# Optimization experiments

Measured on AMD Instinct MI355X. Metric: run time of the kernel, lower is better.

The kernel has to match this reference:

```python
import jax, jax.numpy as jnp
import numpy as np

N, E, G = 30000, 240000, 1000
F, H = 78, 10            # in-features, GAT heads
HID = F * H              # 780
NEG_SLOPE = 0.2


def setup_inputs() -> dict:
    key = jax.random.key(0)
    ks = jax.random.split(key, 12)
    x = jax.random.normal(ks[0], (N, F), dtype=jnp.float32)
    edge_index = jax.random.randint(ks[1], (2, E), 0, N, dtype=jnp.int32)
    batch = jnp.sort(jax.random.randint(ks[2], (N,), 0, G, dtype=jnp.int32))
    def lin(k, fan_in, shape):
        return (jax.random.normal(k, shape, dtype=jnp.float32)
                / jnp.sqrt(jnp.float32(fan_in)))
    return {
        "x": x,
        "edge_index": edge_index,
        "batch": batch,
        "W_gat": lin(ks[3], F, (F, HID)),          # GATConv lin weight
        "att_src": lin(ks[4], F, (H, F)),          # GAT attention vectors
        "att_dst": lin(ks[5], F, (H, F)),
        "b_gat": jnp.zeros((HID,), jnp.float32),
        "W_gcn": lin(ks[6], HID, (HID, HID)),
        "b_gcn": jnp.zeros((HID,), jnp.float32),
        "W1": lin(ks[7], 2 * HID, (2 * HID, 1500)),
        "b1": jnp.zeros((1500,), jnp.float32),
        "W2": lin(ks[8], 1500, (1500, 128)),
        "b2": jnp.zeros((128,), jnp.float32),
    }


def _with_self_loops(edge_index):
    loop = jnp.arange(N, dtype=edge_index.dtype)
    src = jnp.concatenate([edge_index[0], loop])
    dst = jnp.concatenate([edge_index[1], loop])
    return src, dst


def reference(x, edge_index, batch, W_gat, att_src, att_dst, b_gat,
              W_gcn, b_gcn, W1, b1, W2, b2):
    src, dst = _with_self_loops(edge_index)  # [E+N]

    # ---- GATConv(78 -> 78, heads=10, concat) ----
    h = (x @ W_gat).reshape(N, H, F)                       # [N,H,F]
    a_src = jnp.einsum('nhf,hf->nh', h, att_src)           # [N,H]
    a_dst = jnp.einsum('nhf,hf->nh', h, att_dst)
    e = jax.nn.leaky_relu(a_src[src] + a_dst[dst], NEG_SLOPE)  # [Et,H]
    # segment softmax over incoming edges of each dst node
    e_max = jax.ops.segment_max(e, dst, num_segments=N)
    e_exp = jnp.exp(e - e_max[dst])
    denom = jax.ops.segment_sum(e_exp, dst, num_segments=N)
    alpha = e_exp / denom[dst]                             # [Et,H]
    msg = h[src] * alpha[:, :, None]                       # [Et,H,F]
    out = jax.ops.segment_sum(msg, dst, num_segments=N).reshape(N, HID) + b_gat
    out = jax.nn.relu(out)

    # ---- GCNConv(780 -> 780), symmetric norm with self loops ----
    h2 = out @ W_gcn                                       # [N,HID]
    deg = jax.ops.segment_sum(jnp.ones_like(dst, jnp.float32), dst,
                              num_segments=N)
    dinv = jax.lax.rsqrt(jnp.maximum(deg, 1.0))
    norm = dinv[src] * dinv[dst]                           # [Et]
    out2 = jax.ops.segment_sum(norm[:, None] * h2[src], dst,
                               num_segments=N) + b_gcn
    out2 = jax.nn.relu(out2)

    # ---- global mean / max pool over molecules ----
    counts = jax.ops.segment_sum(jnp.ones((N,), jnp.float32), batch,
                                 num_segments=G)
    gsum = jax.ops.segment_sum(out2, batch, num_segments=G)
    gmean = gsum / jnp.maximum(counts, 1.0)[:, None]
    gmax = jax.ops.segment_max(out2, batch, num_segments=G)
    gmax = jnp.where(counts[:, None] > 0, gmax, 0.0)
    pooled = jnp.concatenate([gmean, gmax], axis=1)        # [G, 1560]

    # ---- MLP head (dropout = identity at eval) ----
    hidfc = jax.nn.relu(pooled @ W1 + b1)
    return hidfc @ W2 + b2                                 # [G, 128]
```

## Files before the change

kernel.cpp:

```cpp
#include <hip/hip_runtime.h>

#define NN 30000
#define EE 240000
#define ET 270000
#define GG 1000
#define NH 10
#define FF 78
#define HID 780
#define NEG_SLOPE 0.2f

#define LD_H 784
#define KP_GCN 832
#define NP_HID 896
#define KP_X 96
#define MP_N 30080
#define KP_P 1568
#define NP_W1 1536
#define LD_FC 1504
#define MP_G 1024

#define MT 128
#define NT 128
#define NBLK 30

typedef __bf16 bf16_8 __attribute__((ext_vector_type(8)));
typedef float f32x4 __attribute__((ext_vector_type(4)));

__device__ __forceinline__ void async_copy16(const void* g, void* l) {
  __builtin_amdgcn_global_load_lds(
      (const __attribute__((address_space(1))) void*)g,
      (__attribute__((address_space(3))) void*)l, 16, 0, 0);
}

__device__ __forceinline__ float bf2f(unsigned int bits) {
  return __uint_as_float(bits << 16);
}

__global__ void init_kernel(int* __restrict__ cnt, int* __restrict__ fill,
                            int* __restrict__ lo, int* __restrict__ hi) {
  int i = blockIdx.x * blockDim.x + threadIdx.x;
  if (i < NN) { cnt[i] = 0; fill[i] = 0; }
  if (i < GG) { lo[i] = NN; hi[i] = 0; }
}

template <bool OUT_BF, int KBC>
__global__ __launch_bounds__(256) void mfma_gemm(
    const __bf16* __restrict__ A, const __bf16* __restrict__ BT,
    float* __restrict__ Cf, __bf16* __restrict__ Cb,
    const float* __restrict__ bias, int M, int Kp, int Nout, int ldc,
    int relu, int rp, int nct, int mtiles) {
  constexpr int NCH = KBC / 8;
  constexpr int TST = KBC / 16;
  constexpr int NST = KBC / 32;
  __shared__ __bf16 As[NCH][MT][8];
  __shared__ __bf16 Bs[NCH][NT][8];
  int rt, ct;
  if (rp > 0) {
    int bid = blockIdx.x;
    int p = bid & 7, s = bid >> 3;
    int q = s / nct;
    rt = p * rp + q;
    ct = s - q * nct;
    if (rt >= mtiles) return;
  } else {
    rt = blockIdx.y; ct = blockIdx.x;
  }
  int row0 = rt * MT, col0 = ct * NT;
  int tid = threadIdx.x;
  int lane = tid & 63, wave = tid >> 6;
  int wm = (wave & 1) * 64, wn = (wave >> 1) * 64;
  int l15 = lane & 15, quad = lane >> 4;
  f32x4 acc[4][4] = {};

  for (int k0 = 0; k0 < Kp; k0 += KBC) {
    for (int t = 0; t < TST; t++) {
      int base = t * 256 + wave * 64;
      int s = base + lane;
      int kc = s >> 7, r = s & 127;
      const __bf16* g = A + (size_t)(row0 + r) * Kp + k0 + kc * 8;
      async_copy16(g, (char*)&As[0][0][0] + (size_t)base * 16);
    }
    for (int t = 0; t < TST; t++) {
      int base = t * 256 + wave * 64;
      int s = base + lane;
      int kc = s >> 7, r = s & 127;
      const __bf16* g = BT + (size_t)(col0 + r) * Kp + k0 + kc * 8;
      async_copy16(g, (char*)&Bs[0][0][0] + (size_t)base * 16);
    }
    __syncthreads();

    bf16_8 af[NST][4], bfv[NST][4];
    for (int st = 0; st < NST; st++) {
      for (int mt = 0; mt < 4; mt++)
        af[st][mt] = *(const bf16_8*)&As[st * 4 + quad][wm + mt * 16 + l15][0];
      for (int nt = 0; nt < 4; nt++)
        bfv[st][nt] = *(const bf16_8*)&Bs[st * 4 + quad][wn + nt * 16 + l15][0];
    }
    for (int st = 0; st < NST; st++)
      for (int mt = 0; mt < 4; mt++)
        for (int nt = 0; nt < 4; nt++)
          acc[mt][nt] = __builtin_amdgcn_mfma_f32_16x16x32_bf16(
              af[st][mt], bfv[st][nt], acc[mt][nt], 0, 0, 0);
    __syncthreads();
  }

  for (int nt = 0; nt < 4; nt++) {
    int col = col0 + wn + nt * 16 + l15;
    if (col >= ldc) continue;
    bool valid = col < Nout;
    float bv = (valid && bias) ? bias[col] : 0.f;
    for (int mt = 0; mt < 4; mt++) {
      int rbase = row0 + wm + mt * 16 + quad * 4;
      for (int r = 0; r < 4; r++) {
        int row = rbase + r;
        if (row >= M) continue;
        float v = 0.f;
        if (valid) {
          v = acc[mt][nt][r] + bv;
          if (relu) v = fmaxf(v, 0.f);
        }
        if (OUT_BF) Cb[(size_t)row * ldc + col] = (__bf16)v;
        else        Cf[(size_t)row * ldc + col] = v;
      }
    }
  }
}

__global__ void wconvT_kernel(const float* __restrict__ W,
                              __bf16* __restrict__ BT, int K, int N, int Kp,
                              int Np) {
  int i = blockIdx.x * blockDim.x + threadIdx.x;
  if (i >= Np * Kp) return;
  int n = i / Kp, k = i - n * Kp;
  BT[i] = (__bf16)((n < N && k < K) ? W[(size_t)k * N + n] : 0.f);
}

__global__ void xconv_kernel(const float* __restrict__ x,
                             __bf16* __restrict__ xb) {
  int i = blockIdx.x * blockDim.x + threadIdx.x;
  if (i >= MP_N * KP_X) return;
  int n = i / KP_X, k = i - n * KP_X;
  xb[i] = (__bf16)((n < NN && k < FF) ? x[(size_t)n * FF + k] : 0.f);
}

__global__ void wsd_kernel(const float* __restrict__ W_gat,
                           const float* __restrict__ att_src,
                           const float* __restrict__ att_dst,
                           float* __restrict__ wsd) {
  int i = blockIdx.x * blockDim.x + threadIdx.x;
  if (i >= FF * 2 * NH) return;
  int k = i / (2 * NH), c = i - k * (2 * NH);
  int h = (c < NH) ? c : c - NH;
  const float* att = (c < NH) ? att_src : att_dst;
  float s = 0.f;
  for (int f = 0; f < FF; f++)
    s += W_gat[(size_t)k * HID + h * FF + f] * att[h * FF + f];
  wsd[k * 2 * NH + c] = s;
}

__global__ __launch_bounds__(256) void adot_kernel(
    const float* __restrict__ x, const float* __restrict__ wsd,
    float* __restrict__ a_src, float* __restrict__ a_dst) {
  __shared__ float w_s[FF * 2 * NH];
  for (int i = threadIdx.x; i < FF * 2 * NH; i += 256) w_s[i] = wsd[i];
  __syncthreads();
  int gid = blockIdx.x * 256 + threadIdx.x;
  if (gid >= NN * 2 * NH) return;
  int n = gid / (2 * NH), c = gid - n * (2 * NH);
  float s = 0.f;
  for (int k = 0; k < FF; k++) s += x[(size_t)n * FF + k] * w_s[k * 2 * NH + c];
  if (c < NH) a_src[n * NH + c] = s;
  else        a_dst[n * NH + (c - NH)] = s;
}

__device__ __forceinline__ void edge_sd(const int* __restrict__ ei, int t,
                                        int& s, int& d) {
  if (t < EE) { s = ei[t]; d = ei[EE + t]; }
  else        { s = t - EE; d = t - EE; }
}

__global__ void count_kernel(const int* __restrict__ ei,
                             const int* __restrict__ batch,
                             int* __restrict__ cnt, int* __restrict__ lo,
                             int* __restrict__ hi) {
  int t = blockIdx.x * blockDim.x + threadIdx.x;
  if (t < ET) { int s, d; edge_sd(ei, t, s, d); atomicAdd(&cnt[d], 1); }
  if (t < NN) {
    int g = batch[t];
    atomicMin(&lo[g], t);
    atomicMax(&hi[g], t + 1);
  }
}

__global__ __launch_bounds__(1024) void scan1_kernel(
    const int* __restrict__ cnt, int* __restrict__ row_ptr,
    int* __restrict__ partial) {
  __shared__ int buf[1024];
  int i = blockIdx.x * 1024 + threadIdx.x;
  int v = (i < NN) ? cnt[i] : 0;
  buf[threadIdx.x] = v;
  __syncthreads();
  for (int off = 1; off < 1024; off <<= 1) {
    int t = (threadIdx.x >= off) ? buf[threadIdx.x - off] : 0;
    __syncthreads();
    buf[threadIdx.x] += t;
    __syncthreads();
  }
  if (i < NN) row_ptr[i] = buf[threadIdx.x] - v;
  if (threadIdx.x == 1023) partial[blockIdx.x] = buf[1023];
}

__global__ void scan2_kernel(int* __restrict__ partial,
                             int* __restrict__ offs) {
  if (threadIdx.x == 0) {
    int run = 0;
    for (int b = 0; b < NBLK; b++) { offs[b] = run; run += partial[b]; }
  }
}

__global__ void scan3_kernel(int* __restrict__ row_ptr,
                             const int* __restrict__ offs,
                             const int* __restrict__ cnt,
                             float* __restrict__ dinv) {
  int i = blockIdx.x * blockDim.x + threadIdx.x;
  if (i < NN) {
    row_ptr[i] += offs[i >> 10];
    dinv[i] = rsqrtf((float)max(cnt[i], 1));
  }
  if (i == 0) row_ptr[NN] = ET;
}

__global__ void scatter_kernel(const int* __restrict__ ei,
                               const int* __restrict__ row_ptr,
                               int* __restrict__ fill,
                               const float* __restrict__ a_src,
                               const float* __restrict__ a_dst,
                               int* __restrict__ col_src,
                               float* __restrict__ p_csr) {
  int t = blockIdx.x * blockDim.x + threadIdx.x;
  if (t >= ET) return;
  int s, d; edge_sd(ei, t, s, d);
  int pos = row_ptr[d] + atomicAdd(&fill[d], 1);
  col_src[pos] = s;
#pragma unroll
  for (int h = 0; h < NH; h++) {
    float v = a_src[s * NH + h] + a_dst[d * NH + h];
    v = (v > 0.f) ? v : v * NEG_SLOPE;
    p_csr[(size_t)pos * NH + h] = __expf(v);
  }
}

__global__ __launch_bounds__(256) void gat_aggr_kernel(
    const int* __restrict__ row_ptr, const int* __restrict__ col_src,
    const float* __restrict__ p_csr, const __bf16* __restrict__ h_bf,
    const float* __restrict__ b_gat, __bf16* __restrict__ A_bf) {
  int wave = threadIdx.x >> 6;
  int lane = threadIdx.x & 63;
  int d = blockIdx.x * 4 + wave;
  int beg = row_ptr[d], end = row_ptr[d + 1];
  int f0 = 16 * lane;

  if (lane < 49) {
    int h0 = f0 / FF;
    int split = (h0 + 1) * FF - f0;
    if (split > 16) split = 16;
    int h1 = (h0 < NH - 1) ? h0 + 1 : NH - 1;
    float acc[16] = {};
    float sum0 = 0.f, sum1 = 0.f;
    for (int e = beg; e < end; e++) {
      int s = col_src[e];
      float p0 = p_csr[(size_t)e * NH + h0];
      float p1 = p_csr[(size_t)e * NH + h1];
      sum0 += p0; sum1 += p1;
      const __bf16* rowp = h_bf + (size_t)s * LD_H + f0;
      uint4 r0 = *(const uint4*)rowp;
      uint4 r1 = *(const uint4*)(rowp + 8);
      unsigned int w[8] = {r0.x, r0.y, r0.z, r0.w, r1.x, r1.y, r1.z, r1.w};
#pragma unroll
      for (int k = 0; k < 16; k++) {
        unsigned int bits = (k & 1) ? (w[k >> 1] >> 16) : (w[k >> 1] & 0xffffu);
        acc[k] += bf2f(bits) * ((k < split) ? p0 : p1);
      }
    }
    float inv0 = 1.f / sum0, inv1 = 1.f / sum1;
    bf16_8 o0, o1;
#pragma unroll
    for (int k = 0; k < 16; k++) {
      int f = f0 + k;
      float val = 0.f;
      if (f < HID)
        val = fmaxf(acc[k] * ((k < split) ? inv0 : inv1) + b_gat[f], 0.f);
      if (k < 8) o0[k] = (__bf16)val; else o1[k - 8] = (__bf16)val;
    }
    *(bf16_8*)(A_bf + (size_t)d * KP_GCN + f0) = o0;
    *(bf16_8*)(A_bf + (size_t)d * KP_GCN + f0 + 8) = o1;
  } else if (lane < 52) {
    bf16_8 z = {};
    *(bf16_8*)(A_bf + (size_t)d * KP_GCN + f0) = z;
    *(bf16_8*)(A_bf + (size_t)d * KP_GCN + f0 + 8) = z;
  }
}

__global__ __launch_bounds__(256) void gcn_aggr_kernel(
    const int* __restrict__ row_ptr, const int* __restrict__ col_src,
    const float* __restrict__ dinv, const __bf16* __restrict__ h2,
    const float* __restrict__ b_gcn, __bf16* __restrict__ out2) {
  int wave = threadIdx.x >> 6;
  int lane = threadIdx.x & 63;
  int d = blockIdx.x * 4 + wave;
  int beg = row_ptr[d], end = row_ptr[d + 1];
  if (lane >= 49) return;
  int f0 = 16 * lane;
  float dv = dinv[d];
  float acc[16] = {};
  for (int e = beg; e < end; e++) {
    int s = col_src[e];
    float w = dinv[s] * dv;
    const __bf16* rowp = h2 + (size_t)s * LD_H + f0;
    uint4 r0 = *(const uint4*)rowp;
    uint4 r1 = *(const uint4*)(rowp + 8);
    unsigned int wb[8] = {r0.x, r0.y, r0.z, r0.w, r1.x, r1.y, r1.z, r1.w};
#pragma unroll
    for (int k = 0; k < 16; k++) {
      unsigned int bits = (k & 1) ? (wb[k >> 1] >> 16) : (wb[k >> 1] & 0xffffu);
      acc[k] += bf2f(bits) * w;
    }
  }
  bf16_8 o0, o1;
#pragma unroll
  for (int k = 0; k < 16; k++) {
    int f = f0 + k;
    float val = (f < HID) ? fmaxf(acc[k] + b_gcn[f], 0.f) : 0.f;
    if (k < 8) o0[k] = (__bf16)val; else o1[k - 8] = (__bf16)val;
  }
  *(bf16_8*)(out2 + (size_t)d * LD_H + f0) = o0;
  *(bf16_8*)(out2 + (size_t)d * LD_H + f0 + 8) = o1;
}

__global__ __launch_bounds__(128) void pool_kernel(
    const __bf16* __restrict__ out2, const int* __restrict__ lo,
    const int* __restrict__ hi, __bf16* __restrict__ pooled) {
  int g = blockIdx.x;
  int l = lo[g], h = hi[g];
  int t = threadIdx.x;
  if (t == 98) {
    for (int k = 0; k < 8; k++) pooled[(size_t)g * KP_P + 1560 + k] = (__bf16)0.f;
    return;
  }
  if (t >= 98) return;
  int f0 = 8 * t;
  float s[8] = {}, mx[8];
#pragma unroll
  for (int k = 0; k < 8; k++) mx[k] = -1e30f;
  for (int n = l; n < h; n++) {
    uint4 r = *(const uint4*)(out2 + (size_t)n * LD_H + f0);
    unsigned int w[4] = {r.x, r.y, r.z, r.w};
#pragma unroll
    for (int k = 0; k < 8; k++) {
      unsigned int bits = (k & 1) ? (w[k >> 1] >> 16) : (w[k >> 1] & 0xffffu);
      float v = bf2f(bits);
      s[k] += v;
      mx[k] = fmaxf(mx[k], v);
    }
  }
  float invc = (h > l) ? 1.f / (float)(h - l) : 0.f;
#pragma unroll
  for (int k = 0; k < 8; k++) {
    int f = f0 + k;
    if (f >= HID) continue;
    float mean = (h > l) ? s[k] * invc : 0.f;
    float mxx  = (h > l) ? mx[k] : 0.f;
    pooled[(size_t)g * KP_P + f] = (__bf16)mean;
    pooled[(size_t)g * KP_P + HID + f] = (__bf16)mxx;
  }
}

extern "C" void kernel_launch(void* const* d_in, const int* in_sizes, int n_in,
                              void* d_out, int out_size, void* d_ws,
                              size_t ws_size, hipStream_t stream) {
  const float* x        = (const float*)d_in[0];
  const int*   edge_idx = (const int*)d_in[1];
  const int*   batch    = (const int*)d_in[2];
  const float* W_gat    = (const float*)d_in[3];
  const float* att_src  = (const float*)d_in[4];
  const float* att_dst  = (const float*)d_in[5];
  const float* b_gat    = (const float*)d_in[6];
  const float* W_gcn    = (const float*)d_in[7];
  const float* b_gcn    = (const float*)d_in[8];
  const float* W1       = (const float*)d_in[9];
  const float* b1       = (const float*)d_in[10];
  const float* W2       = (const float*)d_in[11];
  const float* b2       = (const float*)d_in[12];
  float* out = (float*)d_out;
  (void)in_sizes; (void)n_in; (void)out_size; (void)ws_size;

  char* ws = (char*)d_ws;
  size_t off = 0;
  auto alloc = [&](size_t bytes) -> void* {
    void* p = ws + off;
    off += (bytes + 255) & ~(size_t)255;
    return p;
  };
  char*  bufR     = (char*)alloc((size_t)MP_N * KP_GCN * 2);
  __bf16* A_bf    = (__bf16*)bufR;
  __bf16* out2b   = (__bf16*)bufR;
  __bf16* h_bf    = (__bf16*)alloc((size_t)MP_N * LD_H * 2);
  __bf16* h2_bf   = (__bf16*)alloc((size_t)MP_N * LD_H * 2);
  __bf16* x_bf    = (__bf16*)alloc((size_t)MP_N * KP_X * 2);
  __bf16* WgatT   = (__bf16*)alloc((size_t)NP_HID * KP_X * 2);
  __bf16* WgcnT   = (__bf16*)alloc((size_t)NP_HID * KP_GCN * 2);
  __bf16* W1T     = (__bf16*)alloc((size_t)NP_W1 * KP_P * 2);
  __bf16* W2T     = (__bf16*)alloc((size_t)128 * LD_FC * 2);
  __bf16* pooled  = (__bf16*)alloc((size_t)MP_G * KP_P * 2);
  __bf16* hidfc   = (__bf16*)alloc((size_t)MP_G * LD_FC * 2);
  float* wsd      = (float*)alloc((size_t)FF * 2 * NH * 4);
  float* a_src_b  = (float*)alloc((size_t)NN * NH * 4);
  float* a_dst_b  = (float*)alloc((size_t)NN * NH * 4);
  float* p_csr    = (float*)alloc((size_t)ET * NH * 4);
  int*   cnt      = (int*)alloc((size_t)NN * 4);
  int*   fill     = (int*)alloc((size_t)NN * 4);
  int*   row_ptr  = (int*)alloc((size_t)(NN + 1) * 4);
  int*   col_src  = (int*)alloc((size_t)ET * 4);
  int*   partial  = (int*)alloc((size_t)NBLK * 4);
  int*   offs     = (int*)alloc((size_t)NBLK * 4);
  int*   lo       = (int*)alloc((size_t)GG * 4);
  int*   hi       = (int*)alloc((size_t)GG * 4);
  float* dinv     = (float*)alloc((size_t)NN * 4);

  init_kernel<<<(NN + 255) / 256, 256, 0, stream>>>(cnt, fill, lo, hi);

  xconv_kernel<<<(MP_N * KP_X + 255) / 256, 256, 0, stream>>>(x, x_bf);
  wconvT_kernel<<<(NP_HID * KP_X + 255) / 256, 256, 0, stream>>>(
      W_gat, WgatT, FF, HID, KP_X, NP_HID);
  wconvT_kernel<<<(NP_HID * KP_GCN + 255) / 256, 256, 0, stream>>>(
      W_gcn, WgcnT, HID, HID, KP_GCN, NP_HID);
  wconvT_kernel<<<(NP_W1 * KP_P + 255) / 256, 256, 0, stream>>>(
      W1, W1T, 2 * HID, 1500, KP_P, NP_W1);
  wconvT_kernel<<<(128 * LD_FC + 255) / 256, 256, 0, stream>>>(
      W2, W2T, 1500, 128, LD_FC, 128);
  wsd_kernel<<<(FF * 2 * NH + 255) / 256, 256, 0, stream>>>(
      W_gat, att_src, att_dst, wsd);

  {
    dim3 grid(NP_HID / NT, MP_N / MT);
    mfma_gemm<true, 32><<<grid, 256, 0, stream>>>(
        x_bf, WgatT, nullptr, h_bf, nullptr, NN, KP_X, HID, LD_H, 0, 0, 0, 0);
  }
  adot_kernel<<<(NN * 2 * NH + 255) / 256, 256, 0, stream>>>(x, wsd, a_src_b,
                                                             a_dst_b);

  count_kernel<<<(ET + 255) / 256, 256, 0, stream>>>(edge_idx, batch, cnt, lo,
                                                     hi);
  scan1_kernel<<<NBLK, 1024, 0, stream>>>(cnt, row_ptr, partial);
  scan2_kernel<<<1, 64, 0, stream>>>(partial, offs);
  scan3_kernel<<<(NN + 255) / 256, 256, 0, stream>>>(row_ptr, offs, cnt, dinv);
  scatter_kernel<<<(ET + 255) / 256, 256, 0, stream>>>(
      edge_idx, row_ptr, fill, a_src_b, a_dst_b, col_src, p_csr);

  gat_aggr_kernel<<<NN / 4, 256, 0, stream>>>(row_ptr, col_src, p_csr, h_bf,
                                              b_gat, A_bf);
  {
    mfma_gemm<true, 64><<<dim3(8 * 30 * 7), 256, 0, stream>>>(
        A_bf, WgcnT, nullptr, h2_bf, nullptr, NN, KP_GCN, HID, LD_H, 0,
        30, 7, MP_N / MT);
  }
  gcn_aggr_kernel<<<NN / 4, 256, 0, stream>>>(row_ptr, col_src, dinv, h2_bf,
                                              b_gcn, out2b);

  pool_kernel<<<GG, 128, 0, stream>>>(out2b, lo, hi, pooled);

  {
    dim3 grid(NP_W1 / NT, MP_G / MT);
    mfma_gemm<true, 32><<<grid, 256, 0, stream>>>(
        pooled, W1T, nullptr, hidfc, b1, GG, KP_P, 1500, LD_FC, 1, 0, 0, 0);
  }
  {
    dim3 grid(1, MP_G / MT);
    mfma_gemm<false, 32><<<grid, 256, 0, stream>>>(
        hidfc, W2T, out, nullptr, b2, GG, LD_FC, 128, 128, 0, 0, 0, 0);
  }
}
```

Baseline: 631.2 us.

## Fuse prep kernels, stage GEMM epilogue through LDS, batch gathers in aggregation

Merges the conversion, transpose, attention-weight and init kernels into one prep launch to cut launch overhead. The bf16 GEMM epilogue now writes through a swizzled LDS tile so global stores are 16-byte vectors, and the MFMA inner loop keeps fragments for one K step at a time. Both aggregation kernels unroll edges by four so several row gathers are in flight at once. K tile sizes are retuned per GEMM, with padding raised so K stays a multiple of 64. The cost is more register pressure and a larger fixed LDS allocation.

Result: faster. 605.7 us (-4.0%).

```diff
diff --git a/kernel.cpp b/kernel.cpp
--- a/kernel.cpp
+++ b/kernel.cpp
@@ -14,14 +14,23 @@
 #define NP_HID 896
 #define KP_X 96
 #define MP_N 30080
-#define KP_P 1568
+#define KP_P 1600
 #define NP_W1 1536
-#define LD_FC 1504
+#define LD_FC 1536
 #define MP_G 1024
 
 #define MT 128
 #define NT 128
 #define NBLK 30
+
+#define C_X   (MP_N * KP_X)
+#define C_WG  (NP_HID * KP_X)
+#define C_WC  (NP_HID * KP_GCN)
+#define C_W1  (NP_W1 * KP_P)
+#define C_W2  (128 * LD_FC)
+#define C_WS  (FF * 2 * NH)
+#define C_IN  NN
+#define C_TOT (C_X + C_WG + C_WC + C_W1 + C_W2 + C_WS + C_IN)
 
 typedef __bf16 bf16_8 __attribute__((ext_vector_type(8)));
 typedef float f32x4 __attribute__((ext_vector_type(4)));
@@ -34,13 +43,6 @@
 
 __device__ __forceinline__ float bf2f(unsigned int bits) {
   return __uint_as_float(bits << 16);
-}
-
-__global__ void init_kernel(int* __restrict__ cnt, int* __restrict__ fill,
-                            int* __restrict__ lo, int* __restrict__ hi) {
-  int i = blockIdx.x * blockDim.x + threadIdx.x;
-  if (i < NN) { cnt[i] = 0; fill[i] = 0; }
-  if (i < GG) { lo[i] = NN; hi[i] = 0; }
 }
 
 template <bool OUT_BF, int KBC>
@@ -52,8 +54,11 @@
   constexpr int NCH = KBC / 8;
   constexpr int TST = KBC / 16;
   constexpr int NST = KBC / 32;
-  __shared__ __bf16 As[NCH][MT][8];
-  __shared__ __bf16 Bs[NCH][NT][8];
+  constexpr int STAGE = 2 * NCH * MT * 8 * 2;
+  constexpr int SMEM = (STAGE > 32768) ? STAGE : 32768;
+  __shared__ char smem[SMEM];
+  __bf16 (*As)[MT][8] = (__bf16 (*)[MT][8])smem;
+  __bf16 (*Bs)[MT][8] = (__bf16 (*)[MT][8])(smem + (size_t)NCH * MT * 8 * 2);
   int rt, ct;
   if (rp > 0) {
     int bid = blockIdx.x;
@@ -89,73 +94,126 @@
     }
     __syncthreads();
 
-    bf16_8 af[NST][4], bfv[NST][4];
     for (int st = 0; st < NST; st++) {
+      bf16_8 af[4], bfv[4];
       for (int mt = 0; mt < 4; mt++)
-        af[st][mt] = *(const bf16_8*)&As[st * 4 + quad][wm + mt * 16 + l15][0];
+        af[mt] = *(const bf16_8*)&As[st * 4 + quad][wm + mt * 16 + l15][0];
       for (int nt = 0; nt < 4; nt++)
-        bfv[st][nt] = *(const bf16_8*)&Bs[st * 4 + quad][wn + nt * 16 + l15][0];
-    }
-    for (int st = 0; st < NST; st++)
+        bfv[nt] = *(const bf16_8*)&Bs[st * 4 + quad][wn + nt * 16 + l15][0];
       for (int mt = 0; mt < 4; mt++)
         for (int nt = 0; nt < 4; nt++)
           acc[mt][nt] = __builtin_amdgcn_mfma_f32_16x16x32_bf16(
-              af[st][mt], bfv[st][nt], acc[mt][nt], 0, 0, 0);
+              af[mt], bfv[nt], acc[mt][nt], 0, 0, 0);
+    }
     __syncthreads();
   }
 
-  for (int nt = 0; nt < 4; nt++) {
-    int col = col0 + wn + nt * 16 + l15;
-    if (col >= ldc) continue;
-    bool valid = col < Nout;
-    float bv = (valid && bias) ? bias[col] : 0.f;
-    for (int mt = 0; mt < 4; mt++) {
-      int rbase = row0 + wm + mt * 16 + quad * 4;
-      for (int r = 0; r < 4; r++) {
-        int row = rbase + r;
-        if (row >= M) continue;
-        float v = 0.f;
-        if (valid) {
-          v = acc[mt][nt][r] + bv;
-          if (relu) v = fmaxf(v, 0.f);
+  if (OUT_BF) {
+    __bf16* Cs = (__bf16*)smem;
+    for (int nt = 0; nt < 4; nt++) {
+      int col_l = wn + nt * 16 + l15;
+      int gcol = col0 + col_l;
+      bool valid = gcol < Nout;
+      float bv = (valid && bias) ? bias[gcol] : 0.f;
+      int ch = col_l >> 3, wi = col_l & 7;
+      for (int mt = 0; mt < 4; mt++) {
+        for (int r = 0; r < 4; r++) {
+          int rl = wm + mt * 16 + quad * 4 + r;
+          float v = 0.f;
+          if (valid) {
+            v = acc[mt][nt][r] + bv;
+            if (relu) v = fmaxf(v, 0.f);
+          }
+          Cs[rl * 128 + ((ch ^ (rl & 7)) << 3) + wi] = (__bf16)v;
         }
-        if (OUT_BF) Cb[(size_t)row * ldc + col] = (__bf16)v;
-        else        Cf[(size_t)row * ldc + col] = v;
       }
     }
-  }
-}
-
-__global__ void wconvT_kernel(const float* __restrict__ W,
-                              __bf16* __restrict__ BT, int K, int N, int Kp,
-                              int Np) {
-  int i = blockIdx.x * blockDim.x + threadIdx.x;
-  if (i >= Np * Kp) return;
-  int n = i / Kp, k = i - n * Kp;
-  BT[i] = (__bf16)((n < N && k < K) ? W[(size_t)k * N + n] : 0.f);
-}
-
-__global__ void xconv_kernel(const float* __restrict__ x,
-                             __bf16* __restrict__ xb) {
-  int i = blockIdx.x * blockDim.x + threadIdx.x;
-  if (i >= MP_N * KP_X) return;
-  int n = i / KP_X, k = i - n * KP_X;
-  xb[i] = (__bf16)((n < NN && k < FF) ? x[(size_t)n * FF + k] : 0.f);
-}
-
-__global__ void wsd_kernel(const float* __restrict__ W_gat,
-                           const float* __restrict__ att_src,
-                           const float* __restrict__ att_dst,
-                           float* __restrict__ wsd) {
-  int i = blockIdx.x * blockDim.x + threadIdx.x;
-  if (i >= FF * 2 * NH) return;
-  int k = i / (2 * NH), c = i - k * (2 * NH);
-  int h = (c < NH) ? c : c - NH;
-  const float* att = (c < NH) ? att_src : att_dst;
-  float s = 0.f;
-  for (int f = 0; f < FF; f++)
-    s += W_gat[(size_t)k * HID + h * FF + f] * att[h * FF + f];
-  wsd[k * 2 * NH + c] = s;
+    __syncthreads();
+    for (int idx = tid; idx < MT * 16; idx += 256) {
+      int rl = idx >> 4, ch = idx & 15;
+      int grow = row0 + rl, gcol = col0 + ch * 8;
+      if (grow < M && gcol + 8 <= ldc)
+        *(bf16_8*)(Cb + (size_t)grow * ldc + gcol) =
+            *(const bf16_8*)&Cs[rl * 128 + ((ch ^ (rl & 7)) << 3)];
+    }
+  } else {
+    for (int nt = 0; nt < 4; nt++) {
+      int col = col0 + wn + nt * 16 + l15;
+      if (col >= ldc) continue;
+      bool valid = col < Nout;
+      float bv = (valid && bias) ? bias[col] : 0.f;
+      for (int mt = 0; mt < 4; mt++) {
+        int rbase = row0 + wm + mt * 16 + quad * 4;
+        for (int r = 0; r < 4; r++) {
+          int row = rbase + r;
+          if (row >= M) continue;
+          float v = 0.f;
+          if (valid) {
+            v = acc[mt][nt][r] + bv;
+            if (relu) v = fmaxf(v, 0.f);
+          }
+          Cf[(size_t)row * ldc + col] = v;
+        }
+      }
+    }
+  }
+}
+
+__global__ __launch_bounds__(256) void prep_kernel(
+    const float* __restrict__ x, const float* __restrict__ W_gat,
+    const float* __restrict__ att_src, const float* __restrict__ att_dst,
+    const float* __restrict__ W_gcn, const float* __restrict__ W1,
+    const float* __restrict__ W2, __bf16* __restrict__ x_bf,
+    __bf16* __restrict__ WgatT, __bf16* __restrict__ WgcnT,
+    __bf16* __restrict__ W1T, __bf16* __restrict__ W2T,
+    float* __restrict__ wsd, int* __restrict__ cnt, int* __restrict__ fill,
+    int* __restrict__ lo, int* __restrict__ hi) {
+  int gid = blockIdx.x * 256 + threadIdx.x;
+  if (gid < C_X) {
+    int n = gid / KP_X, k = gid - n * KP_X;
+    x_bf[gid] = (__bf16)((n < NN && k < FF) ? x[(size_t)n * FF + k] : 0.f);
+    return;
+  }
+  gid -= C_X;
+  if (gid < C_WG) {
+    int n = gid / KP_X, k = gid - n * KP_X;
+    WgatT[gid] = (__bf16)((n < HID && k < FF) ? W_gat[(size_t)k * HID + n] : 0.f);
+    return;
+  }
+  gid -= C_WG;
+  if (gid < C_WC) {
+    int n = gid / KP_GCN, k = gid - n * KP_GCN;
+    WgcnT[gid] = (__bf16)((n < HID && k < HID) ? W_gcn[(size_t)k * HID + n] : 0.f);
+    return;
+  }
+  gid -= C_WC;
+  if (gid < C_W1) {
+    int n = gid / KP_P, k = gid - n * KP_P;
+    W1T[gid] = (__bf16)((n < 1500 && k < 2 * HID) ? W1[(size_t)k * 1500 + n] : 0.f);
+    return;
+  }
+  gid -= C_W1;
+  if (gid < C_W2) {
+    int n = gid / LD_FC, k = gid - n * LD_FC;
+    W2T[gid] = (__bf16)((n < 128 && k < 1500) ? W2[(size_t)k * 128 + n] : 0.f);
+    return;
+  }
+  gid -= C_W2;
+  if (gid < C_WS) {
+    int k = gid / (2 * NH), c = gid - k * (2 * NH);
+    int h = (c < NH) ? c : c - NH;
+    const float* att = (c < NH) ? att_src : att_dst;
+    float s = 0.f;
+    for (int f = 0; f < FF; f++)
+      s += W_gat[(size_t)k * HID + h * FF + f] * att[h * FF + f];
+    wsd[k * 2 * NH + c] = s;
+    return;
+  }
+  gid -= C_WS;
+  if (gid < C_IN) {
+    cnt[gid] = 0; fill[gid] = 0;
+    if (gid < GG) { lo[gid] = NN; hi[gid] = 0; }
+  }
 }
 
 __global__ __launch_bounds__(256) void adot_kernel(
@@ -267,19 +325,35 @@
     int h1 = (h0 < NH - 1) ? h0 + 1 : NH - 1;
     float acc[16] = {};
     float sum0 = 0.f, sum1 = 0.f;
-    for (int e = beg; e < end; e++) {
-      int s = col_src[e];
-      float p0 = p_csr[(size_t)e * NH + h0];
-      float p1 = p_csr[(size_t)e * NH + h1];
-      sum0 += p0; sum1 += p1;
-      const __bf16* rowp = h_bf + (size_t)s * LD_H + f0;
-      uint4 r0 = *(const uint4*)rowp;
-      uint4 r1 = *(const uint4*)(rowp + 8);
-      unsigned int w[8] = {r0.x, r0.y, r0.z, r0.w, r1.x, r1.y, r1.z, r1.w};
-#pragma unroll
-      for (int k = 0; k < 16; k++) {
-        unsigned int bits = (k & 1) ? (w[k >> 1] >> 16) : (w[k >> 1] & 0xffffu);
-        acc[k] += bf2f(bits) * ((k < split) ? p0 : p1);
+    for (int e = beg; e < end; e += 4) {
+      int sidx[4]; float pp0[4], pp1[4];
+#pragma unroll
+      for (int j = 0; j < 4; j++) {
+        bool ok = (e + j < end);
+        int ee = ok ? e + j : beg;
+        sidx[j] = col_src[ee];
+        float q0 = p_csr[(size_t)ee * NH + h0];
+        float q1 = p_csr[(size_t)ee * NH + h1];
+        pp0[j] = ok ? q0 : 0.f;
+        pp1[j] = ok ? q1 : 0.f;
+      }
+      uint4 rr0[4], rr1[4];
+#pragma unroll
+      for (int j = 0; j < 4; j++) {
+        const __bf16* rowp = h_bf + (size_t)sidx[j] * LD_H + f0;
+        rr0[j] = *(const uint4*)rowp;
+        rr1[j] = *(const uint4*)(rowp + 8);
+      }
+#pragma unroll
+      for (int j = 0; j < 4; j++) {
+        sum0 += pp0[j]; sum1 += pp1[j];
+        unsigned int w[8] = {rr0[j].x, rr0[j].y, rr0[j].z, rr0[j].w,
+                             rr1[j].x, rr1[j].y, rr1[j].z, rr1[j].w};
+#pragma unroll
+        for (int k = 0; k < 16; k++) {
+          unsigned int bits = (k & 1) ? (w[k >> 1] >> 16) : (w[k >> 1] & 0xffffu);
+          acc[k] += bf2f(bits) * ((k < split) ? pp0[j] : pp1[j]);
+        }
       }
     }
     float inv0 = 1.f / sum0, inv1 = 1.f / sum1;
@@ -313,17 +387,32 @@
   int f0 = 16 * lane;
   float dv = dinv[d];
   float acc[16] = {};
-  for (int e = beg; e < end; e++) {
-    int s = col_src[e];
-    float w = dinv[s] * dv;
-    const __bf16* rowp = h2 + (size_t)s * LD_H + f0;
-    uint4 r0 = *(const uint4*)rowp;
-    uint4 r1 = *(const uint4*)(rowp + 8);
-    unsigned int wb[8] = {r0.x, r0.y, r0.z, r0.w, r1.x, r1.y, r1.z, r1.w};
-#pragma unroll
-    for (int k = 0; k < 16; k++) {
-      unsigned int bits = (k & 1) ? (wb[k >> 1] >> 16) : (wb[k >> 1] & 0xffffu);
-      acc[k] += bf2f(bits) * w;
+  for (int e = beg; e < end; e += 4) {
+    int sidx[4]; float ww[4];
+#pragma unroll
+    for (int j = 0; j < 4; j++) {
+      bool ok = (e + j < end);
+      int ee = ok ? e + j : beg;
+      int s = col_src[ee];
+      sidx[j] = s;
+      ww[j] = ok ? dinv[s] * dv : 0.f;
+    }
+    uint4 rr0[4], rr1[4];
+#pragma unroll
+    for (int j = 0; j < 4; j++) {
+      const __bf16* rowp = h2 + (size_t)sidx[j] * LD_H + f0;
+      rr0[j] = *(const uint4*)rowp;
+      rr1[j] = *(const uint4*)(rowp + 8);
+    }
+#pragma unroll
+    for (int j = 0; j < 4; j++) {
+      unsigned int wb[8] = {rr0[j].x, rr0[j].y, rr0[j].z, rr0[j].w,
+                            rr1[j].x, rr1[j].y, rr1[j].z, rr1[j].w};
+#pragma unroll
+      for (int k = 0; k < 16; k++) {
+        unsigned int bits = (k & 1) ? (wb[k >> 1] >> 16) : (wb[k >> 1] & 0xffffu);
+        acc[k] += bf2f(bits) * ww[j];
+      }
     }
   }
   bf16_8 o0, o1;
@@ -343,11 +432,13 @@
   int g = blockIdx.x;
   int l = lo[g], h = hi[g];
   int t = threadIdx.x;
-  if (t == 98) {
-    for (int k = 0; k < 8; k++) pooled[(size_t)g * KP_P + 1560 + k] = (__bf16)0.f;
-    return;
-  }
-  if (t >= 98) return;
+  if (t >= 98) {
+    if (t < 103) {
+      int base = 1560 + (t - 98) * 8;
+      for (int k = 0; k < 8; k++) pooled[(size_t)g * KP_P + base + k] = (__bf16)0.f;
+    }
+    return;
+  }
   int f0 = 8 * t;
   float s[8] = {}, mx[8];
 #pragma unroll
@@ -427,19 +518,9 @@
   int*   hi       = (int*)alloc((size_t)GG * 4);
   float* dinv     = (float*)alloc((size_t)NN * 4);
 
-  init_kernel<<<(NN + 255) / 256, 256, 0, stream>>>(cnt, fill, lo, hi);
-
-  xconv_kernel<<<(MP_N * KP_X + 255) / 256, 256, 0, stream>>>(x, x_bf);
-  wconvT_kernel<<<(NP_HID * KP_X + 255) / 256, 256, 0, stream>>>(
-      W_gat, WgatT, FF, HID, KP_X, NP_HID);
-  wconvT_kernel<<<(NP_HID * KP_GCN + 255) / 256, 256, 0, stream>>>(
-      W_gcn, WgcnT, HID, HID, KP_GCN, NP_HID);
-  wconvT_kernel<<<(NP_W1 * KP_P + 255) / 256, 256, 0, stream>>>(
-      W1, W1T, 2 * HID, 1500, KP_P, NP_W1);
-  wconvT_kernel<<<(128 * LD_FC + 255) / 256, 256, 0, stream>>>(
-      W2, W2T, 1500, 128, LD_FC, 128);
-  wsd_kernel<<<(FF * 2 * NH + 255) / 256, 256, 0, stream>>>(
-      W_gat, att_src, att_dst, wsd);
+  prep_kernel<<<(C_TOT + 255) / 256, 256, 0, stream>>>(
+      x, W_gat, att_src, att_dst, W_gcn, W1, W2, x_bf, WgatT, WgcnT, W1T, W2T,
+      wsd, cnt, fill, lo, hi);
 
   {
     dim3 grid(NP_HID / NT, MP_N / MT);
@@ -460,7 +541,7 @@
   gat_aggr_kernel<<<NN / 4, 256, 0, stream>>>(row_ptr, col_src, p_csr, h_bf,
                                               b_gat, A_bf);
   {
-    mfma_gemm<true, 64><<<dim3(8 * 30 * 7), 256, 0, stream>>>(
+    mfma_gemm<true, 32><<<dim3(8 * 30 * 7), 256, 0, stream>>>(
         A_bf, WgcnT, nullptr, h2_bf, nullptr, NN, KP_GCN, HID, LD_H, 0,
         30, 7, MP_N / MT);
   }
@@ -471,12 +552,12 @@
 
   {
     dim3 grid(NP_W1 / NT, MP_G / MT);
-    mfma_gemm<true, 32><<<grid, 256, 0, stream>>>(
+    mfma_gemm<true, 64><<<grid, 256, 0, stream>>>(
         pooled, W1T, nullptr, hidfc, b1, GG, KP_P, 1500, LD_FC, 1, 0, 0, 0);
   }
   {
     dim3 grid(1, MP_G / MT);
-    mfma_gemm<false, 32><<<grid, 256, 0, stream>>>(
+    mfma_gemm<false, 64><<<grid, 256, 0, stream>>>(
         hidfc, W2T, out, nullptr, b2, GG, LD_FC, 128, 128, 0, 0, 0, 0);
   }
 }
```
